# Performance work log

Hardware: AMD Instinct MI355X
Metric: run time of the kernel (lower is better)

## Reference

```python
import jax, jax.numpy as jnp
import numpy as np

T_STEPS, B, DX, DH = 512, 64, 1024, 1024


def setup_inputs() -> dict:
    key = jax.random.key(0)
    ks = jax.random.split(key, 8)
    s_in = 1.0 / np.sqrt(DX)
    s_h = 1.0 / np.sqrt(DH)
    return {
        "xs": jax.random.normal(ks[0], (T_STEPS, B, DX), jnp.float32),
        "ms": jax.random.normal(ks[1], (T_STEPS, B, DH), jnp.float32),
        "h0": jnp.zeros((B, DH), jnp.float32),
        "W_ih": jax.random.normal(ks[2], (3 * DH, DX), jnp.float32) * s_in,
        "b_ih": jnp.zeros((3 * DH,), jnp.float32),
        "W_hh": jax.random.normal(ks[3], (3 * DH, DH), jnp.float32) * s_h,
        "b_hh": jnp.zeros((3 * DH,), jnp.float32),
        "W_xh": jax.random.normal(ks[4], (DH, DX), jnp.float32) * s_in,
        "b_xh": jnp.zeros((DH,), jnp.float32),
        "W_r": jax.random.normal(ks[5], (DH, DH), jnp.float32) * s_h,
        "b_r": jnpp if False else jnp.zeros((DH,), jnp.float32),
    }


def reference(xs, ms, h0, W_ih, b_ih, W_hh, b_hh, W_xh, b_xh, W_r, b_r):
    # Precompute all input-side projections in one big GEMM each (same math,
    # just hoisted out of the recurrent loop).
    xg = jnp.einsum('tbd,gd->tbg', xs, W_ih) + b_ih          # [T,B,3*Dh]
    xh = jnp.einsum('tbd,hd->tbh', xs, W_xh) + b_xh          # [T,B,Dh]
    tm = jnp.tanh(ms)                                        # [T,B,Dh]

    def step(h, inp):
        xg_t, xh_t, tm_t = inp
        hg = h @ W_hh.T + b_hh                               # [B,3*Dh]
        gates = jax.nn.sigmoid(xg_t + hg)
        rt, zt, et = jnp.split(gates, 3, axis=-1)
        ht_hat = jnp.tanh(xh_t + (rt * h) @ W_r.T + b_r)
        ht = zt * h + (1.0 - zt) * ht_hat + et * tm_t
        return ht, ht

    h_last, outs = jax.lax.scan(step, h0, (xg, xh, tm))
    return outs, h_last
```

## Files before the change

kernel.cpp:

```cpp
#include <hip/hip_runtime.h>
#include <stdint.h>

#define TSTEPS 512

typedef __attribute__((ext_vector_type(8))) _Float16 half8;
typedef __attribute__((ext_vector_type(4))) _Float16 half4;
typedef __attribute__((ext_vector_type(4))) float f32x4;
typedef __attribute__((ext_vector_type(4))) float float4v;
typedef unsigned long long u64;

static __device__ __forceinline__ float sigm(float x) { return 1.f / (1.f + __expf(-x)); }
static __device__ __forceinline__ float tanh_(float x) {
  x = fminf(15.f, fmaxf(-15.f, x));
  float e = __expf(-2.f * x);
  return (1.f - e) / (1.f + e);
}
static __device__ __forceinline__ half8 ld8(const _Float16* p) { return *(const half8*)p; }
static __device__ __forceinline__ f32x4 MFMA(half8 a, half8 b, f32x4 c) {
  return __builtin_amdgcn_mfma_f32_16x16x32_f16(a, b, c, 0, 0, 0);
}

struct U64x2 { u64 x, y; };
static __device__ __forceinline__ half8 ld_msg16(const u64* p) {
  u64 a = __hip_atomic_load(p,     __ATOMIC_RELAXED, __HIP_MEMORY_SCOPE_AGENT);
  u64 b = __hip_atomic_load(p + 1, __ATOMIC_RELAXED, __HIP_MEMORY_SCOPE_AGENT);
  U64x2 u{a, b};
  return __builtin_bit_cast(half8, u);
}
static __device__ __forceinline__ void st_msg8(u64* p, u64 v) {
  __hip_atomic_store(p, v, __ATOMIC_RELAXED, __HIP_MEMORY_SCOPE_AGENT);
}

__global__ __launch_bounds__(256) void kconv(
    const float* __restrict__ xs, const float* __restrict__ wih,
    const float* __restrict__ wxh, const float* __restrict__ whhf,
    const float* __restrict__ wrf, const float* __restrict__ h0,
    _Float16* __restrict__ xs_h, _Float16* __restrict__ wcat,
    _Float16* __restrict__ whh, _Float16* __restrict__ wr,
    _Float16* __restrict__ hx) {
  const long n1 = 8388608;
  const long n2 = 1048576;
  const long n3 = 786432;
  const long n4 = 262144;
  const long n5 = 16384;
  const long total = n1 + n2 + n3 + n4 + n5;
  for (long i = (long)blockIdx.x * 256 + threadIdx.x; i < total; i += (long)gridDim.x * 256) {
    const float* s; _Float16* d;
    if (i < n1) { s = xs + i * 4; d = xs_h + i * 4; }
    else if (i < n1 + n2) {
      long e = (i - n1) * 4;
      s = (e < 3145728) ? (wih + e) : (wxh + (e - 3145728));
      d = wcat + e;
    } else if (i < n1 + n2 + n3) { long e = (i - n1 - n2) * 4; s = whhf + e; d = whh + e; }
    else if (i < n1 + n2 + n3 + n4) { long e = (i - n1 - n2 - n3) * 4; s = wrf + e; d = wr + e; }
    else { long e = (i - n1 - n2 - n3 - n4) * 4; s = h0 + e; d = hx + e; }
    float4v v = *(const float4v*)s;
    half4 o = { (_Float16)v.x, (_Float16)v.y, (_Float16)v.z, (_Float16)v.w };
    *(half4*)d = o;
  }
}

__global__ __launch_bounds__(256) void kgemm(
    const _Float16* __restrict__ X, const _Float16* __restrict__ W,
    const float* __restrict__ b_ih, const float* __restrict__ b_xh,
    _Float16* __restrict__ C) {
  __shared__ _Float16 As[128 * 40], Bs[128 * 40];
  const int tid = threadIdx.x;
  const int lane = tid & 63;
  const int w = tid >> 6;
  const int wm = (w >> 1) * 64, wn = (w & 1) * 64;
  const int bn = blockIdx.x * 128;
  const int bm = blockIdx.y * 128;
  const int arow = tid >> 2;
  const int kk8 = (tid & 3) * 8;
  const int fr = lane & 15, fq = lane >> 4;
  const f32x4 zero = {0.f, 0.f, 0.f, 0.f};
  f32x4 acc[4][4];
  #pragma unroll
  for (int a = 0; a < 4; a++)
    #pragma unroll
    for (int b = 0; b < 4; b++) acc[a][b] = zero;
  for (int kt = 0; kt < 1024; kt += 32) {
    __syncthreads();
    #pragma unroll
    for (int j = 0; j < 2; j++) {
      int r = j * 64 + arow;
      *(half8*)(As + r * 40 + kk8) = ld8(X + (size_t)(bm + r) * 1024 + kt + kk8);
      *(half8*)(Bs + r * 40 + kk8) = ld8(W + (size_t)(bn + r) * 1024 + kt + kk8);
    }
    __syncthreads();
    half8 af[4], bfr[4];
    #pragma unroll
    for (int i = 0; i < 4; i++) {
      af[i]  = *(const half8*)(As + (wm + i * 16 + fr) * 40 + fq * 8);
      bfr[i] = *(const half8*)(Bs + (wn + i * 16 + fr) * 40 + fq * 8);
    }
    #pragma unroll
    for (int mi = 0; mi < 4; mi++)
      #pragma unroll
      for (int ni = 0; ni < 4; ni++)
        acc[mi][ni] = MFMA(af[mi], bfr[ni], acc[mi][ni]);
  }
  #pragma unroll
  for (int mi = 0; mi < 4; mi++)
    #pragma unroll
    for (int ni = 0; ni < 4; ni++) {
      int col = bn + wn + ni * 16 + fr;
      float bias = (col < 3072) ? b_ih[col] : b_xh[col - 3072];
      #pragma unroll
      for (int r = 0; r < 4; r++) {
        int row = bm + wm + mi * 16 + fq * 4 + r;
        C[(size_t)row * 4096 + col] = (_Float16)(acc[mi][ni][r] + bias);
      }
    }
}

static __device__ __forceinline__ void bar_arrive(unsigned* bp) {
  asm volatile("s_waitcnt vmcnt(0)" ::: "memory");
  __syncthreads();
  if (threadIdx.x == 0)
    __hip_atomic_fetch_add(bp, 1u, __ATOMIC_RELAXED, __HIP_MEMORY_SCOPE_AGENT);
}
static __device__ __forceinline__ void bar_wait(unsigned* bp, unsigned tgt) {
  if (threadIdx.x == 0)
    while (__hip_atomic_load(bp, __ATOMIC_RELAXED, __HIP_MEMORY_SCOPE_AGENT) < tgt)
      __builtin_amdgcn_s_sleep(1);
  __syncthreads();
  asm volatile("" ::: "memory");
}

#define TP 272
#define RP 17

__global__ __launch_bounds__(512) void krec(
    const _Float16* __restrict__ xgh, const float* __restrict__ ms,
    const _Float16* __restrict__ whh, const _Float16* __restrict__ wr,
    const float* __restrict__ b_hh, const float* __restrict__ b_r,
    const float* __restrict__ h0,
    _Float16* __restrict__ hx, _Float16* __restrict__ rhx,
    float* __restrict__ out, unsigned* __restrict__ ctr) {
  __shared__ float red[48 * TP];
  __shared__ _Float16 hsh[512];
  const int tid = threadIdx.x;
  const int lane = tid & 63, w = tid >> 6;
  const int fr = lane & 15, fq = lane >> 4;
  const int g = (int)blockIdx.x >> 5;
  const int colbase = ((int)blockIdx.x & 31) * 32;
  unsigned* bar = ctr + g * 64;

  half8 wA[6][4], wB[2][4];
  #pragma unroll
  for (int nt = 0; nt < 6; nt++)
    #pragma unroll
    for (int ks = 0; ks < 4; ks++)
      wA[nt][ks] = ld8(whh + (size_t)((nt >> 1) * 1024 + colbase + (nt & 1) * 16 + fr) * 1024
                            + w * 128 + ks * 32 + fq * 8);
  #pragma unroll
  for (int nt = 0; nt < 2; nt++)
    #pragma unroll
    for (int ks = 0; ks < 4; ks++)
      wB[nt][ks] = ld8(wr + (size_t)(colbase + nt * 16 + fr) * 1024
                           + w * 128 + ks * 32 + fq * 8);

  const int b = tid >> 5, cc = tid & 31;
  const int gc = colbase + cc;
  const int gm = g * 16 + b;
  const float bhr = b_hh[gc], bhz = b_hh[1024 + gc], bhe = b_hh[2048 + gc];
  const float brr = b_r[gc];
  float hreg = h0[(size_t)gm * 1024 + gc];

  const u64* hx64  = (const u64*)hx  + (((g * 16 + fr) * 1024 + w * 128 + fq * 8) >> 2);
  const u64* rhx64 = (const u64*)rhx + (((g * 16 + fr) * 1024 + w * 128 + fq * 8) >> 2);
  u64* hpub  = (u64*)hx  + (((g * 16 + (tid >> 3)) * 1024 + colbase + (tid & 7) * 4) >> 2);
  u64* rhpub = (u64*)rhx + (((g * 16 + (tid >> 3)) * 1024 + colbase + (tid & 7) * 4) >> 2);
  const _Float16* hsrc = hsh + (tid >> 3) * 32 + (tid & 7) * 4;

  const f32x4 zero = {0.f, 0.f, 0.f, 0.f};

  float pxr, pxz, pxe, pxh, ptm;
  {
    const _Float16* xp = xgh + (size_t)gm * 4096;
    pxr = (float)xp[gc]; pxz = (float)xp[1024 + gc];
    pxe = (float)xp[2048 + gc]; pxh = (float)xp[3072 + gc];
    ptm = tanh_(ms[(size_t)gm * 1024 + gc]);
  }

  #pragma clang loop unroll(disable)
  for (int t = 0; t < TSTEPS; t++) {
    half8 av[4];
    if (t == 0) {
      #pragma unroll
      for (int ks = 0; ks < 4; ks++)
        av[ks] = ld8(hx + (g * 16 + fr) * 1024 + w * 128 + ks * 32 + fq * 8);
    } else {
      #pragma unroll
      for (int ks = 0; ks < 4; ks++)
        av[ks] = ld_msg16(hx64 + ks * 8);
    }
    f32x4 accA[6];
    #pragma unroll
    for (int nt = 0; nt < 6; nt++) accA[nt] = zero;
    #pragma unroll
    for (int ks = 0; ks < 4; ks++)
      #pragma unroll
      for (int nt = 0; nt < 6; nt++)
        accA[nt] = MFMA(av[ks], wA[nt][ks], accA[nt]);
    #pragma unroll
    for (int nt = 0; nt < 6; nt++)
      #pragma unroll
      for (int r = 0; r < 4; r++)
        red[(w * 6 + nt) * TP + (fq * 4 + r) * RP + fr] = accA[nt][r];
    __syncthreads();
    float sr = pxr + bhr, sz = pxz + bhz, se = pxe + bhe;
    {
      const int boff = b * RP + (cc & 15) + (cc >> 4) * TP;
      #pragma unroll
      for (int w8 = 0; w8 < 8; w8++) {
        const float* rp = red + w8 * 6 * TP + boff;
        sr += rp[0]; sz += rp[2 * TP]; se += rp[4 * TP];
      }
    }
    float rg = sigm(sr);
    float zz = sigm(sz), ee = sigm(se);
    hsh[tid] = (_Float16)(rg * hreg);
    __syncthreads();
    if (tid < 128)
      st_msg8(rhpub, __builtin_bit_cast(u64, *(const half4*)hsrc));
    bar_arrive(bar);
    float nxr = 0.f, nxz = 0.f, nxe = 0.f, nxh = 0.f, ntm = 0.f;
    if (t + 1 < TSTEPS) {
      const _Float16* xp = xgh + (size_t)((t + 1) * 64 + gm) * 4096;
      nxr = (float)xp[gc]; nxz = (float)xp[1024 + gc];
      nxe = (float)xp[2048 + gc]; nxh = (float)xp[3072 + gc];
      ntm = tanh_(ms[(size_t)(t + 1) * 65536 + gm * 1024 + gc]);
    }
    bar_wait(bar, (unsigned)(64 * t + 32));

    half8 bv[4];
    #pragma unroll
    for (int ks = 0; ks < 4; ks++)
      bv[ks] = ld_msg16(rhx64 + ks * 8);
    f32x4 accB[2];
    #pragma unroll
    for (int nt = 0; nt < 2; nt++) accB[nt] = zero;
    #pragma unroll
    for (int ks = 0; ks < 4; ks++)
      #pragma unroll
      for (int nt = 0; nt < 2; nt++)
        accB[nt] = MFMA(bv[ks], wB[nt][ks], accB[nt]);
    __syncthreads();
    #pragma unroll
    for (int nt = 0; nt < 2; nt++)
      #pragma unroll
      for (int r = 0; r < 4; r++)
        red[(w * 6 + nt) * TP + (fq * 4 + r) * RP + fr] = accB[nt][r];
    __syncthreads();
    float s = pxh + brr;
    {
      const int boff = b * RP + (cc & 15) + (cc >> 4) * TP;
      #pragma unroll
      for (int w8 = 0; w8 < 8; w8++) s += red[w8 * 6 * TP + boff];
    }
    float hh = tanh_(s);
    float hn = zz * hreg + (1.f - zz) * hh + ee * ptm;
    hreg = hn;
    out[(size_t)t * 65536 + gm * 1024 + gc] = hn;
    hsh[tid] = (_Float16)hn;
    __syncthreads();
    if (tid < 128)
      st_msg8(hpub, __builtin_bit_cast(u64, *(const half4*)hsrc));
    bar_arrive(bar);
    bar_wait(bar, (unsigned)(64 * t + 64));
    pxr = nxr; pxz = nxz; pxe = nxe; pxh = nxh; ptm = ntm;
  }
  out[(size_t)TSTEPS * 65536 + gm * 1024 + gc] = hreg;
}

extern "C" void kernel_launch(void* const* d_in, const int* in_sizes, int n_in,
                              void* d_out, int out_size, void* d_ws, size_t ws_size,
                              hipStream_t stream) {
  const float* xs   = (const float*)d_in[0];
  const float* ms   = (const float*)d_in[1];
  const float* h0   = (const float*)d_in[2];
  const float* W_ih = (const float*)d_in[3];
  const float* b_ih = (const float*)d_in[4];
  const float* W_hh = (const float*)d_in[5];
  const float* b_hh = (const float*)d_in[6];
  const float* W_xh = (const float*)d_in[7];
  const float* b_xh = (const float*)d_in[8];
  const float* W_r  = (const float*)d_in[9];
  const float* b_r  = (const float*)d_in[10];

  char* ws = (char*)d_ws;
  size_t off = 0;
  _Float16* xs_h = (_Float16*)(ws + off); off += 67108864;
  _Float16* wcat = (_Float16*)(ws + off); off += 8388608;
  _Float16* whh  = (_Float16*)(ws + off); off += 6291456;
  _Float16* wr   = (_Float16*)(ws + off); off += 2097152;
  _Float16* xgh  = (_Float16*)(ws + off); off += 268435456;
  _Float16* hx   = (_Float16*)(ws + off); off += 131072;
  _Float16* rhx  = (_Float16*)(ws + off); off += 131072;
  unsigned* ctr  = (unsigned*)(ws + off); off += 1024;

  hipMemsetAsync(ctr, 0, 1024, stream);
  kconv<<<2048, 256, 0, stream>>>(xs, W_ih, W_xh, W_hh, W_r, h0,
                                  xs_h, wcat, whh, wr, hx);
  kgemm<<<dim3(32, 256), 256, 0, stream>>>(xs_h, wcat, b_ih, b_xh, xgh);
  krec<<<128, 512, 0, stream>>>(xgh, ms, whh, wr, b_hh, b_r, h0,
                                hx, rhx, (float*)d_out, ctr);
}
```

Baseline: 4.432 ms.

## Replace atomic-counter group barrier with per-block flag arrays and double-buffered h exchange

The fetch-add counter barriers between the 32 blocks of each batch group are replaced by per-block flag slots. Each block stores its step number to its own slot, and waiters poll all 32 slots with one wave using __all. The hidden-state and r*h exchange buffers are double-buffered by step parity, which removes the trailing barrier at the end of each step and one __syncthreads. This is meant to cut serialized atomic contention and barrier latency on the recurrent critical path. It relies on correct parity indexing: at t=0 the kernel reads hx buffer 0, which kconv fills with h0. It also doubles the exchange-buffer workspace.

```diff
diff --git a/kernel.cpp b/kernel.cpp
--- a/kernel.cpp
+++ b/kernel.cpp
@@ -29,6 +29,11 @@
 }
 static __device__ __forceinline__ void st_msg8(u64* p, u64 v) {
   __hip_atomic_store(p, v, __ATOMIC_RELAXED, __HIP_MEMORY_SCOPE_AGENT);
+}
+static __device__ __forceinline__ void wait_flags(const unsigned* line, unsigned tag) {
+  const unsigned* p = line + (threadIdx.x & 31);
+  while (!__all(__hip_atomic_load(p, __ATOMIC_RELAXED, __HIP_MEMORY_SCOPE_AGENT) >= tag))
+    __builtin_amdgcn_s_sleep(1);
 }
 
 __global__ __launch_bounds__(256) void kconv(
@@ -115,24 +120,10 @@
     }
 }
 
-static __device__ __forceinline__ void bar_arrive(unsigned* bp) {
-  asm volatile("s_waitcnt vmcnt(0)" ::: "memory");
-  __syncthreads();
-  if (threadIdx.x == 0)
-    __hip_atomic_fetch_add(bp, 1u, __ATOMIC_RELAXED, __HIP_MEMORY_SCOPE_AGENT);
-}
-static __device__ __forceinline__ void bar_wait(unsigned* bp, unsigned tgt) {
-  if (threadIdx.x == 0)
-    while (__hip_atomic_load(bp, __ATOMIC_RELAXED, __HIP_MEMORY_SCOPE_AGENT) < tgt)
-      __builtin_amdgcn_s_sleep(1);
-  __syncthreads();
-  asm volatile("" ::: "memory");
-}
-
 #define TP 272
 #define RP 17
 
-__global__ __launch_bounds__(512) void krec(
+__global__ __launch_bounds__(512, 2) void krec(
     const _Float16* __restrict__ xgh, const float* __restrict__ ms,
     const _Float16* __restrict__ whh, const _Float16* __restrict__ wr,
     const float* __restrict__ b_hh, const float* __restrict__ b_r,
@@ -145,8 +136,10 @@
   const int lane = tid & 63, w = tid >> 6;
   const int fr = lane & 15, fq = lane >> 4;
   const int g = (int)blockIdx.x >> 5;
-  const int colbase = ((int)blockIdx.x & 31) * 32;
-  unsigned* bar = ctr + g * 64;
+  const int slot = (int)blockIdx.x & 31;
+  const int colbase = slot * 32;
+  unsigned* flagA = ctr + (g * 2 + 0) * 32;
+  unsigned* flagB = ctr + (g * 2 + 1) * 32;
 
   half8 wA[6][4], wB[2][4];
   #pragma unroll
@@ -187,16 +180,12 @@
 
   #pragma clang loop unroll(disable)
   for (int t = 0; t < TSTEPS; t++) {
+    const int ph = t & 1;
+    wait_flags(flagB, (unsigned)t);
     half8 av[4];
-    if (t == 0) {
-      #pragma unroll
-      for (int ks = 0; ks < 4; ks++)
-        av[ks] = ld8(hx + (g * 16 + fr) * 1024 + w * 128 + ks * 32 + fq * 8);
-    } else {
-      #pragma unroll
-      for (int ks = 0; ks < 4; ks++)
-        av[ks] = ld_msg16(hx64 + ks * 8);
-    }
+    #pragma unroll
+    for (int ks = 0; ks < 4; ks++)
+      av[ks] = ld_msg16(hx64 + ph * 16384 + ks * 8);
     f32x4 accA[6];
     #pragma unroll
     for (int nt = 0; nt < 6; nt++) accA[nt] = zero;
@@ -224,9 +213,14 @@
     float zz = sigm(sz), ee = sigm(se);
     hsh[tid] = (_Float16)(rg * hreg);
     __syncthreads();
-    if (tid < 128)
-      st_msg8(rhpub, __builtin_bit_cast(u64, *(const half4*)hsrc));
-    bar_arrive(bar);
+    if (tid < 128) {
+      st_msg8(rhpub + ph * 16384, __builtin_bit_cast(u64, *(const half4*)hsrc));
+      asm volatile("s_waitcnt vmcnt(0)" ::: "memory");
+    }
+    __syncthreads();
+    if (tid == 0)
+      __hip_atomic_store(flagA + slot, (unsigned)(t + 1),
+                         __ATOMIC_RELAXED, __HIP_MEMORY_SCOPE_AGENT);
     float nxr = 0.f, nxz = 0.f, nxe = 0.f, nxh = 0.f, ntm = 0.f;
     if (t + 1 < TSTEPS) {
       const _Float16* xp = xgh + (size_t)((t + 1) * 64 + gm) * 4096;
@@ -234,12 +228,12 @@
       nxe = (float)xp[2048 + gc]; nxh = (float)xp[3072 + gc];
       ntm = tanh_(ms[(size_t)(t + 1) * 65536 + gm * 1024 + gc]);
     }
-    bar_wait(bar, (unsigned)(64 * t + 32));
+    wait_flags(flagA, (unsigned)(t + 1));
 
     half8 bv[4];
     #pragma unroll
     for (int ks = 0; ks < 4; ks++)
-      bv[ks] = ld_msg16(rhx64 + ks * 8);
+      bv[ks] = ld_msg16(rhx64 + ph * 16384 + ks * 8);
     f32x4 accB[2];
     #pragma unroll
     for (int nt = 0; nt < 2; nt++) accB[nt] = zero;
@@ -248,7 +242,6 @@
       #pragma unroll
       for (int nt = 0; nt < 2; nt++)
         accB[nt] = MFMA(bv[ks], wB[nt][ks], accB[nt]);
-    __syncthreads();
     #pragma unroll
     for (int nt = 0; nt < 2; nt++)
       #pragma unroll
@@ -267,10 +260,14 @@
     out[(size_t)t * 65536 + gm * 1024 + gc] = hn;
     hsh[tid] = (_Float16)hn;
     __syncthreads();
-    if (tid < 128)
-      st_msg8(hpub, __builtin_bit_cast(u64, *(const half4*)hsrc));
-    bar_arrive(bar);
-    bar_wait(bar, (unsigned)(64 * t + 64));
+    if (tid < 128) {
+      st_msg8(hpub + (ph ^ 1) * 16384, __builtin_bit_cast(u64, *(const half4*)hsrc));
+      asm volatile("s_waitcnt vmcnt(0)" ::: "memory");
+    }
+    __syncthreads();
+    if (tid == 0)
+      __hip_atomic_store(flagB + slot, (unsigned)(t + 1),
+                         __ATOMIC_RELAXED, __HIP_MEMORY_SCOPE_AGENT);
     pxr = nxr; pxz = nxz; pxe = nxe; pxh = nxh; ptm = ntm;
   }
   out[(size_t)TSTEPS * 65536 + gm * 1024 + gc] = hreg;
@@ -298,8 +295,8 @@
   _Float16* whh  = (_Float16*)(ws + off); off += 6291456;
   _Float16* wr   = (_Float16*)(ws + off); off += 2097152;
   _Float16* xgh  = (_Float16*)(ws + off); off += 268435456;
-  _Float16* hx   = (_Float16*)(ws + off); off += 131072;
-  _Float16* rhx  = (_Float16*)(ws + off); off += 131072;
+  _Float16* hx   = (_Float16*)(ws + off); off += 262144;
+  _Float16* rhx  = (_Float16*)(ws + off); off += 262144;
   unsigned* ctr  = (unsigned*)(ws + off); off += 1024;
 
   hipMemsetAsync(ctr, 0, 1024, stream);
```

Result: no change. 4.480 ms (+1.1%).
